# Optimization experiments

Hardware: AMD Instinct MI355X
Metric: run time of the kernel (lower is better)

## Reference

```python
import jax, jax.numpy as jnp
import numpy as np

DROPOUT_RATE = 0.6


def dropout(x, key, rate=DROPOUT_RATE):
    keep = jax.random.bernoulli(key, 1.0 - rate, x.shape)
    return jnp.where(keep, x / (1.0 - rate), 0.0).astype(x.dtype)


def gcn_conv(x, W, b, src, dst, n_nodes):
    # h = x @ W  (tiny linear), then symmetric-normalized scatter-add over edges
    h = x @ W                                             # [N, C_out]
    deg = jax.ops.segment_sum(jnp.ones_like(dst, dtype=h.dtype), dst,
                              num_segments=n_nodes)       # in-degree at targets
    dinv = jnp.where(deg > 0, jax.lax.rsqrt(jnp.maximum(deg, 1.0)), 0.0)
    norm = dinv[src] * dinv[dst]                          # [E]
    msg = h[src] * norm[:, None]                          # [E, C_out] gather
    out = jax.ops.segment_sum(msg, dst, num_segments=n_nodes)  # scatter-add
    return out + b


def setup_inputs() -> dict:
    key = jax.random.key(0)
    k_x, k_e, k_w1, k_w2 = jax.random.split(key, 4)
    N, E = 100000, 6400000
    x = jax.random.normal(k_x, (N, 1), dtype=jnp.float32)
    edge_index = jax.random.randint(k_e, (2, E), 0, N, dtype=jnp.int64)
    # GCNConv weights (glorot-ish scale) and zero biases
    W1 = jax.random.normal(k_w1, (1, 16), dtype=jnp.float32) * (1.0 / np.sqrt(1.0))
    b1 = jnp.zeros((16,), dtype=jnp.float32)
    W2 = jax.random.normal(k_w2, (16, 1), dtype=jnp.float32) * (1.0 / np.sqrt(16.0))
    b2 = jnp.zeros((1,), dtype=jnp.float32)
    return {"x": x, "edge_index": edge_index, "W1": W1, "b1": b1, "W2": W2, "b2": b2}


def reference(x, edge_index, W1, b1, W2, b2):
    n_nodes = x.shape[0]
    src, dst = edge_index[0], edge_index[1]
    k1, k2 = jax.random.split(jax.random.key(42), 2)
    h = dropout(x, k1)
    h = gcn_conv(h, W1, b1, src, dst, n_nodes)
    h = jax.nn.relu(h)
    h = dropout(h, k2)
    out = gcn_conv(h, W2, b2, src, dst, n_nodes)
    return out
```

## Files before the change

### kernel.cpp

```cpp
#include <hip/hip_runtime.h>
#include <hip/hip_bf16.h>
#include <stdint.h>


#define KEEP_P 0.4f
#define RANGE 2048
#define SHIFT 11
#define MASK 2047
#define BPC 512
#define KS 32
#define SEGS (BPC / KS)
#define NBMAX 64

__host__ __device__ inline unsigned rotl32(unsigned v, int s) {
  return (v << s) | (v >> (32 - s));
}

__host__ __device__ inline void threefry2x32(unsigned key0, unsigned key1,
                                             unsigned x0, unsigned x1,
                                             unsigned& o0, unsigned& o1) {
  unsigned ks0 = key0, ks1 = key1, ks2 = key0 ^ key1 ^ 0x1BD11BDAu;
  unsigned v0 = x0 + ks0, v1 = x1 + ks1;
#define TF_R(r) { v0 += v1; v1 = rotl32(v1, r); v1 ^= v0; }
  TF_R(13) TF_R(15) TF_R(26) TF_R(6)
  v0 += ks1; v1 += ks2 + 1u;
  TF_R(17) TF_R(29) TF_R(16) TF_R(24)
  v0 += ks2; v1 += ks0 + 2u;
  TF_R(13) TF_R(15) TF_R(26) TF_R(6)
  v0 += ks0; v1 += ks1 + 3u;
  TF_R(17) TF_R(29) TF_R(16) TF_R(24)
  v0 += ks1; v1 += ks2 + 4u;
  TF_R(13) TF_R(15) TF_R(26) TF_R(6)
  v0 += ks2; v1 += ks0 + 5u;
#undef TF_R
  o0 = v0; o1 = v1;
}

__device__ inline float u01_from_bits(unsigned bits) {
  return __uint_as_float((bits >> 9) | 0x3f800000u) - 1.0f;
}

__global__ __launch_bounds__(256) void k_part(
    const int* __restrict__ src, const int* __restrict__ dst,
    unsigned* __restrict__ slots, unsigned* __restrict__ cnt,
    int NB, int CAP, int e4, int E) {
  __shared__ unsigned cur[NBMAX];
  const int tid = threadIdx.x;
  const size_t blkbase = (size_t)blockIdx.x * NB;
  for (int p = tid; p < NB; p += 256) cur[p] = (unsigned)(p * CAP);
  __syncthreads();
  const int chunk = (e4 + BPC - 1) / BPC;
  const int j0 = blockIdx.x * chunk;
  const int j1 = min(j0 + chunk, e4);
  const int4* dst4 = reinterpret_cast<const int4*>(dst);
  const int4* src4 = reinterpret_cast<const int4*>(src);
  unsigned* myslots = slots + blkbase * CAP;
#define PART_ONE(d, s) { unsigned p = (unsigned)(d) >> SHIFT; \
    unsigned pos = atomicAdd(&cur[p], 1u); \
    myslots[pos] = ((unsigned)(d) & MASK) | ((unsigned)(s) << SHIFT); }
  for (int j = j0 + tid; j < j1; j += 256) {
    int4 d = dst4[j];
    int4 s = src4[j];
    PART_ONE(d.x, s.x) PART_ONE(d.y, s.y) PART_ONE(d.z, s.z) PART_ONE(d.w, s.w)
  }
  if (blockIdx.x == 0) {
    for (int t = e4 * 4 + tid; t < E; t += 256) PART_ONE(dst[t], src[t])
  }
#undef PART_ONE
  __syncthreads();
  for (int p = tid; p < NB; p += 256)
    cnt[blkbase + p] = cur[p] - (unsigned)(p * CAP);
}

__global__ __launch_bounds__(256) void k_deg2(
    const unsigned* __restrict__ slots, const unsigned* __restrict__ cnt,
    unsigned short* __restrict__ part16, int NB, int CAP) {
  __shared__ unsigned bins[RANGE / 2];
  const int tid = threadIdx.x;
  const int p = blockIdx.y, kd = blockIdx.x;
  for (int i = tid; i < RANGE / 2; i += 256) bins[i] = 0u;
  __syncthreads();
  const int b0 = kd * SEGS;
#define DEG_ONE(v) { unsigned r = (v) & MASK; \
    atomicAdd(&bins[r >> 1], 1u << ((r & 1) * 16)); }
  for (int u = 0; u < SEGS / 2; ++u) {
    const int bA = b0 + u, bB = b0 + u + SEGS / 2;
    const int lA = cnt[(size_t)bA * NB + p];
    const int lB = cnt[(size_t)bB * NB + p];
    const unsigned* eA = slots + ((size_t)bA * NB + p) * CAP;
    const unsigned* eB = slots + ((size_t)bB * NB + p) * CAP;
    int jA = tid, jB = tid;
    while (jA < lA && jB < lB) {
      unsigned vA = eA[jA], vB = eB[jB];
      DEG_ONE(vA) DEG_ONE(vB)
      jA += 256; jB += 256;
    }
    for (; jA < lA; jA += 256) DEG_ONE(eA[jA])
    for (; jB < lB; jB += 256) DEG_ONE(eB[jB])
  }
#undef DEG_ONE
  __syncthreads();
  unsigned* my32 = (unsigned*)(part16 + ((size_t)kd * gridDim.y + p) * RANGE);
  for (int i = tid; i < RANGE / 2; i += 256) my32[i] = bins[i];
}

__global__ __launch_bounds__(256) void k_node1(
    const float* __restrict__ x, const unsigned short* __restrict__ part16,
    float* __restrict__ dinv, float* __restrict__ y,
    int NB, int n, unsigned k1a, unsigned k1b) {
  int i = blockIdx.x * blockDim.x + threadIdx.x;
  if (i >= n) return;
  const int p = i >> SHIFT, r = i & MASK;
  unsigned d = 0;
  for (int b = 0; b < KS; ++b)
    d += part16[((size_t)b * NB + p) * RANGE + r];
  float di = (d > 0) ? (1.0f / sqrtf((float)d)) : 0.0f;
  dinv[i] = di;
  unsigned o0, o1;
  threefry2x32(k1a, k1b, 0u, (unsigned)i, o0, o1);
  float u = u01_from_bits(o0 ^ o1);
  float xd = (u < KEEP_P) ? (x[i] / KEEP_P) : 0.0f;
  y[i] = xd * di;
}

__global__ __launch_bounds__(256) void k_scat(
    const unsigned* __restrict__ slots, const unsigned* __restrict__ cnt,
    const float* __restrict__ val, float* __restrict__ part,
    int NB, int CAP) {
  __shared__ float bins[RANGE];
  const int tid = threadIdx.x;
  const int p = blockIdx.y, ks = blockIdx.x;
  for (int i = tid; i < RANGE; i += 256) bins[i] = 0.0f;
  __syncthreads();
  const int b0 = ks * SEGS;
  for (int u = 0; u < SEGS / 2; ++u) {
    const int bA = b0 + u, bB = b0 + u + SEGS / 2;
    const int lA = cnt[(size_t)bA * NB + p];
    const int lB = cnt[(size_t)bB * NB + p];
    const unsigned* eA = slots + ((size_t)bA * NB + p) * CAP;
    const unsigned* eB = slots + ((size_t)bB * NB + p) * CAP;
    int jA = tid, jB = tid;
    while (jA < lA && jB < lB) {
      unsigned vA = eA[jA], vB = eB[jB];
      float aA = val[vA >> SHIFT], aB = val[vB >> SHIFT];
      atomicAdd(&bins[vA & MASK], aA);
      atomicAdd(&bins[vB & MASK], aB);
      jA += 256; jB += 256;
    }
    for (; jA < lA; jA += 256) {
      unsigned v = eA[jA];
      atomicAdd(&bins[v & MASK], val[v >> SHIFT]);
    }
    for (; jB < lB; jB += 256) {
      unsigned v = eB[jB];
      atomicAdd(&bins[v & MASK], val[v >> SHIFT]);
    }
  }
  __syncthreads();
  float* my = part + ((size_t)ks * NB + p) * RANGE;
  for (int i = tid; i < RANGE; i += 256) my[i] = bins[i];
}

__global__ __launch_bounds__(256) void k_node2(
    const float* __restrict__ part, const float* __restrict__ dinv,
    const float* __restrict__ W1, const float* __restrict__ b1,
    const float* __restrict__ W2, float* __restrict__ z2,
    int NB, int n, unsigned k2a, unsigned k2b) {
  int i = blockIdx.x * blockDim.x + threadIdx.x;
  if (i >= n) return;
  const int p = i >> SHIFT, r = i & MASK;
  float s = 0.0f;
  for (int b = 0; b < KS; ++b)
    s += part[((size_t)b * NB + p) * RANGE + r];
  float t = s * dinv[i];
  float z = 0.0f;
  unsigned base = (unsigned)i * 16u;
#pragma unroll
  for (int c = 0; c < 16; ++c) {
    float h = W1[c] * t + b1[c];
    h = fmaxf(h, 0.0f);
    unsigned o0, o1;
    threefry2x32(k2a, k2b, 0u, base + (unsigned)c, o0, o1);
    float u = u01_from_bits(o0 ^ o1);
    float hd = (u < KEEP_P) ? (h / KEEP_P) : 0.0f;
    z += hd * W2[c];
  }
  z2[i] = z * dinv[i];
}

__global__ __launch_bounds__(256) void k_final(
    const float* __restrict__ part, const float* __restrict__ dinv,
    const float* __restrict__ b2, float* __restrict__ out,
    int NB, int n) {
  int i = blockIdx.x * blockDim.x + threadIdx.x;
  if (i >= n) return;
  const int p = i >> SHIFT, r = i & MASK;
  float s = 0.0f;
  for (int b = 0; b < KS; ++b)
    s += part[((size_t)b * NB + p) * RANGE + r];
  out[i] = b2[0] + dinv[i] * s;
}

extern "C" void kernel_launch(void* const* d_in, const int* in_sizes, int n_in,
                              void* d_out, int out_size, void* d_ws, size_t ws_size,
                              hipStream_t stream) {
  const float* x  = (const float*)d_in[0];
  const int* edge = (const int*)d_in[1];
  const float* W1 = (const float*)d_in[2];
  const float* b1 = (const float*)d_in[3];
  const float* W2 = (const float*)d_in[4];
  const float* b2 = (const float*)d_in[5];
  float* out = (float*)d_out;

  const int N = in_sizes[0];
  const int E = in_sizes[1] / 2;
  const int* src = edge;
  const int* dst = edge + E;

  const int NP = (N + 255) & ~255;
  const int NB = (N + RANGE - 1) / RANGE;

  const size_t cnt_sz  = (size_t)BPC * NB * 4;
  const size_t part_sz = (size_t)KS * NB * RANGE * 4;
  const size_t small_sz = (size_t)3 * NP * 4;
  size_t fixed = cnt_sz + part_sz + small_sz + 512;
  size_t avail = ws_size > fixed ? ws_size - fixed : 0;
  int CAP = (int)(avail / ((size_t)NB * BPC * 4));
  if (CAP > 512) CAP = 512;
  if (CAP < 288) CAP = 288;

  char* w = (char*)d_ws;
  unsigned* slots = (unsigned*)w;        w += (size_t)NB * BPC * CAP * 4;
  unsigned* cnt   = (unsigned*)w;        w += cnt_sz;
  w = (char*)(((uintptr_t)w + 255) & ~(uintptr_t)255);
  float* part_f = (float*)w;
  unsigned short* part16 = (unsigned short*)w;
  w += part_sz;
  float* dinv = (float*)w;
  float* y    = dinv + NP;
  float* z2   = y + NP;

  unsigned k1a, k1b, k2a, k2b;
  threefry2x32(0u, 42u, 0u, 0u, k1a, k1b);
  threefry2x32(0u, 42u, 0u, 1u, k2a, k2b);

  const int e4 = E >> 2;
  const int gN = (N + 255) / 256;

  k_part <<<BPC, 256, 0, stream>>>(src, dst, slots, cnt, NB, CAP, e4, E);
  k_deg2 <<<dim3(KS, NB), 256, 0, stream>>>(slots, cnt, part16, NB, CAP);
  k_node1<<<gN, 256, 0, stream>>>(x, part16, dinv, y, NB, N, k1a, k1b);
  k_scat <<<dim3(KS, NB), 256, 0, stream>>>(slots, cnt, y, part_f, NB, CAP);
  k_node2<<<gN, 256, 0, stream>>>(part_f, dinv, W1, b1, W2, z2, NB, N, k2a, k2b);
  k_scat <<<dim3(KS, NB), 256, 0, stream>>>(slots, cnt, z2, part_f, NB, CAP);
  k_final<<<gN, 256, 0, stream>>>(part_f, dinv, b2, out, NB, N);
}
```

Before: 231.5 us.

## Stage partition writes through shared-memory tiles and assign segments per wavefront

The partition kernel now handles edges in tiles of 2048. For each tile it builds a per-bucket histogram, scans it, sorts the tile into shared memory, and then writes each bucket's run to global memory as a contiguous sequence, replacing the old scattered per-edge global stores. The degree and scatter kernels now give each wavefront its own segments and read slot entries with 16-byte vector loads, and CAP is rounded down to a multiple of 4 so those loads stay aligned. The cost is extra syncthreads and shared-memory traffic in the partition kernel, plus possible load imbalance between wavefronts.

```diff
diff --git a/kernel.cpp b/kernel.cpp
--- a/kernel.cpp
+++ b/kernel.cpp
@@ -11,6 +11,8 @@
 #define KS 32
 #define SEGS (BPC / KS)
 #define NBMAX 64
+#define TILE 2048
+#define TILE4 (TILE / 4)
 
 __host__ __device__ inline unsigned rotl32(unsigned v, int s) {
   return (v << s) | (v >> (32 - s));
@@ -44,29 +46,83 @@
     const int* __restrict__ src, const int* __restrict__ dst,
     unsigned* __restrict__ slots, unsigned* __restrict__ cnt,
     int NB, int CAP, int e4, int E) {
-  __shared__ unsigned cur[NBMAX];
+  __shared__ unsigned hist[NBMAX], scan_s[NBMAX + 1], off[NBMAX];
+  __shared__ unsigned tbase[NBMAX], cur[NBMAX];
+  __shared__ unsigned stage[TILE];
+  __shared__ unsigned char stage_p[TILE];
   const int tid = threadIdx.x;
   const size_t blkbase = (size_t)blockIdx.x * NB;
+  unsigned* myslots = slots + blkbase * CAP;
   for (int p = tid; p < NB; p += 256) cur[p] = (unsigned)(p * CAP);
-  __syncthreads();
   const int chunk = (e4 + BPC - 1) / BPC;
   const int j0 = blockIdx.x * chunk;
   const int j1 = min(j0 + chunk, e4);
   const int4* dst4 = reinterpret_cast<const int4*>(dst);
   const int4* src4 = reinterpret_cast<const int4*>(src);
-  unsigned* myslots = slots + blkbase * CAP;
-#define PART_ONE(d, s) { unsigned p = (unsigned)(d) >> SHIFT; \
-    unsigned pos = atomicAdd(&cur[p], 1u); \
-    myslots[pos] = ((unsigned)(d) & MASK) | ((unsigned)(s) << SHIFT); }
-  for (int j = j0 + tid; j < j1; j += 256) {
-    int4 d = dst4[j];
-    int4 s = src4[j];
-    PART_ONE(d.x, s.x) PART_ONE(d.y, s.y) PART_ONE(d.z, s.z) PART_ONE(d.w, s.w)
-  }
+
+  for (int t0 = j0; t0 < j1; t0 += TILE4) {
+    __syncthreads();
+    for (int p = tid; p < NB; p += 256) hist[p] = 0u;
+    __syncthreads();
+    const int ja = t0 + tid, jb = t0 + TILE4 / 2 + tid;
+    const bool va = ja < j1 && tid < TILE4 / 2;
+    const bool vb = jb < j1;
+    int4 da, db;
+    if (va) {
+      da = dst4[ja];
+      atomicAdd(&hist[(unsigned)da.x >> SHIFT], 1u);
+      atomicAdd(&hist[(unsigned)da.y >> SHIFT], 1u);
+      atomicAdd(&hist[(unsigned)da.z >> SHIFT], 1u);
+      atomicAdd(&hist[(unsigned)da.w >> SHIFT], 1u);
+    }
+    if (vb) {
+      db = dst4[jb];
+      atomicAdd(&hist[(unsigned)db.x >> SHIFT], 1u);
+      atomicAdd(&hist[(unsigned)db.y >> SHIFT], 1u);
+      atomicAdd(&hist[(unsigned)db.z >> SHIFT], 1u);
+      atomicAdd(&hist[(unsigned)db.w >> SHIFT], 1u);
+    }
+    __syncthreads();
+    if (tid == 0) {
+      unsigned acc = 0;
+      for (int p = 0; p < NB; ++p) { scan_s[p] = acc; acc += hist[p]; }
+      scan_s[NB] = acc;
+    }
+    __syncthreads();
+    for (int p = tid; p < NB; p += 256) {
+      off[p] = scan_s[p];
+      tbase[p] = cur[p];
+      cur[p] += hist[p];
+    }
+    __syncthreads();
+#define STAGE1(d, s) { unsigned ud = (unsigned)(d), us = (unsigned)(s); \
+    unsigned p = ud >> SHIFT; unsigned pos = atomicAdd(&off[p], 1u); \
+    stage[pos] = (ud & MASK) | (us << SHIFT); stage_p[pos] = (unsigned char)p; }
+    if (va) {
+      int4 sa = src4[ja];
+      STAGE1(da.x, sa.x) STAGE1(da.y, sa.y) STAGE1(da.z, sa.z) STAGE1(da.w, sa.w)
+    }
+    if (vb) {
+      int4 sb = src4[jb];
+      STAGE1(db.x, sb.x) STAGE1(db.y, sb.y) STAGE1(db.z, sb.z) STAGE1(db.w, sb.w)
+    }
+#undef STAGE1
+    __syncthreads();
+    const int tc = (int)scan_s[NB];
+    for (int i = tid; i < tc; i += 256) {
+      unsigned p = stage_p[i];
+      myslots[tbase[p] + ((unsigned)i - scan_s[p])] = stage[i];
+    }
+  }
+  __syncthreads();
   if (blockIdx.x == 0) {
-    for (int t = e4 * 4 + tid; t < E; t += 256) PART_ONE(dst[t], src[t])
-  }
-#undef PART_ONE
+    for (int t = e4 * 4 + tid; t < E; t += 256) {
+      unsigned ud = (unsigned)dst[t], us = (unsigned)src[t];
+      unsigned p = ud >> SHIFT;
+      unsigned pos = atomicAdd(&cur[p], 1u);
+      myslots[pos] = (ud & MASK) | (us << SHIFT);
+    }
+  }
   __syncthreads();
   for (int p = tid; p < NB; p += 256)
     cnt[blkbase + p] = cur[p] - (unsigned)(p * CAP);
@@ -76,27 +132,34 @@
     const unsigned* __restrict__ slots, const unsigned* __restrict__ cnt,
     unsigned short* __restrict__ part16, int NB, int CAP) {
   __shared__ unsigned bins[RANGE / 2];
-  const int tid = threadIdx.x;
+  const int tid = threadIdx.x, w = tid >> 6, lane = tid & 63;
   const int p = blockIdx.y, kd = blockIdx.x;
   for (int i = tid; i < RANGE / 2; i += 256) bins[i] = 0u;
   __syncthreads();
   const int b0 = kd * SEGS;
 #define DEG_ONE(v) { unsigned r = (v) & MASK; \
     atomicAdd(&bins[r >> 1], 1u << ((r & 1) * 16)); }
-  for (int u = 0; u < SEGS / 2; ++u) {
-    const int bA = b0 + u, bB = b0 + u + SEGS / 2;
+  for (int q = 0; q < 4; q += 2) {
+    const int bA = b0 + w + 4 * q, bB = b0 + w + 4 * (q + 1);
     const int lA = cnt[(size_t)bA * NB + p];
     const int lB = cnt[(size_t)bB * NB + p];
     const unsigned* eA = slots + ((size_t)bA * NB + p) * CAP;
     const unsigned* eB = slots + ((size_t)bB * NB + p) * CAP;
-    int jA = tid, jB = tid;
-    while (jA < lA && jB < lB) {
-      unsigned vA = eA[jA], vB = eB[jB];
-      DEG_ONE(vA) DEG_ONE(vB)
-      jA += 256; jB += 256;
-    }
-    for (; jA < lA; jA += 256) DEG_ONE(eA[jA])
-    for (; jB < lB; jB += 256) DEG_ONE(eB[jB])
+    const int lmax = lA > lB ? lA : lB;
+    for (int base = 4 * lane; base < lmax; base += 256) {
+      if (base + 4 <= lA) {
+        uint4 av = *reinterpret_cast<const uint4*>(eA + base);
+        DEG_ONE(av.x) DEG_ONE(av.y) DEG_ONE(av.z) DEG_ONE(av.w)
+      } else {
+        for (int k = base; k < lA; ++k) DEG_ONE(eA[k])
+      }
+      if (base + 4 <= lB) {
+        uint4 bv = *reinterpret_cast<const uint4*>(eB + base);
+        DEG_ONE(bv.x) DEG_ONE(bv.y) DEG_ONE(bv.z) DEG_ONE(bv.w)
+      } else {
+        for (int k = base; k < lB; ++k) DEG_ONE(eB[k])
+      }
+    }
   }
 #undef DEG_ONE
   __syncthreads();
@@ -128,32 +191,65 @@
     const float* __restrict__ val, float* __restrict__ part,
     int NB, int CAP) {
   __shared__ float bins[RANGE];
-  const int tid = threadIdx.x;
+  const int tid = threadIdx.x, w = tid >> 6, lane = tid & 63;
   const int p = blockIdx.y, ks = blockIdx.x;
   for (int i = tid; i < RANGE; i += 256) bins[i] = 0.0f;
   __syncthreads();
   const int b0 = ks * SEGS;
-  for (int u = 0; u < SEGS / 2; ++u) {
-    const int bA = b0 + u, bB = b0 + u + SEGS / 2;
+  for (int q = 0; q < 4; q += 2) {
+    const int bA = b0 + w + 4 * q, bB = b0 + w + 4 * (q + 1);
     const int lA = cnt[(size_t)bA * NB + p];
     const int lB = cnt[(size_t)bB * NB + p];
     const unsigned* eA = slots + ((size_t)bA * NB + p) * CAP;
     const unsigned* eB = slots + ((size_t)bB * NB + p) * CAP;
-    int jA = tid, jB = tid;
-    while (jA < lA && jB < lB) {
-      unsigned vA = eA[jA], vB = eB[jB];
-      float aA = val[vA >> SHIFT], aB = val[vB >> SHIFT];
-      atomicAdd(&bins[vA & MASK], aA);
-      atomicAdd(&bins[vB & MASK], aB);
-      jA += 256; jB += 256;
-    }
-    for (; jA < lA; jA += 256) {
-      unsigned v = eA[jA];
-      atomicAdd(&bins[v & MASK], val[v >> SHIFT]);
-    }
-    for (; jB < lB; jB += 256) {
-      unsigned v = eB[jB];
-      atomicAdd(&bins[v & MASK], val[v >> SHIFT]);
+    const int lmax = lA > lB ? lA : lB;
+    for (int base = 4 * lane; base < lmax; base += 256) {
+      const bool fA = base + 4 <= lA, fB = base + 4 <= lB;
+      if (fA && fB) {
+        uint4 av = *reinterpret_cast<const uint4*>(eA + base);
+        uint4 bv = *reinterpret_cast<const uint4*>(eB + base);
+        float a0 = val[av.x >> SHIFT], a1 = val[av.y >> SHIFT];
+        float a2 = val[av.z >> SHIFT], a3 = val[av.w >> SHIFT];
+        float c0 = val[bv.x >> SHIFT], c1 = val[bv.y >> SHIFT];
+        float c2 = val[bv.z >> SHIFT], c3 = val[bv.w >> SHIFT];
+        atomicAdd(&bins[av.x & MASK], a0);
+        atomicAdd(&bins[av.y & MASK], a1);
+        atomicAdd(&bins[av.z & MASK], a2);
+        atomicAdd(&bins[av.w & MASK], a3);
+        atomicAdd(&bins[bv.x & MASK], c0);
+        atomicAdd(&bins[bv.y & MASK], c1);
+        atomicAdd(&bins[bv.z & MASK], c2);
+        atomicAdd(&bins[bv.w & MASK], c3);
+      } else {
+        if (fA) {
+          uint4 av = *reinterpret_cast<const uint4*>(eA + base);
+          float a0 = val[av.x >> SHIFT], a1 = val[av.y >> SHIFT];
+          float a2 = val[av.z >> SHIFT], a3 = val[av.w >> SHIFT];
+          atomicAdd(&bins[av.x & MASK], a0);
+          atomicAdd(&bins[av.y & MASK], a1);
+          atomicAdd(&bins[av.z & MASK], a2);
+          atomicAdd(&bins[av.w & MASK], a3);
+        } else {
+          for (int k = base; k < lA; ++k) {
+            unsigned v = eA[k];
+            atomicAdd(&bins[v & MASK], val[v >> SHIFT]);
+          }
+        }
+        if (fB) {
+          uint4 bv = *reinterpret_cast<const uint4*>(eB + base);
+          float c0 = val[bv.x >> SHIFT], c1 = val[bv.y >> SHIFT];
+          float c2 = val[bv.z >> SHIFT], c3 = val[bv.w >> SHIFT];
+          atomicAdd(&bins[bv.x & MASK], c0);
+          atomicAdd(&bins[bv.y & MASK], c1);
+          atomicAdd(&bins[bv.z & MASK], c2);
+          atomicAdd(&bins[bv.w & MASK], c3);
+        } else {
+          for (int k = base; k < lB; ++k) {
+            unsigned v = eB[k];
+            atomicAdd(&bins[v & MASK], val[v >> SHIFT]);
+          }
+        }
+      }
     }
   }
   __syncthreads();
@@ -226,6 +322,7 @@
   size_t fixed = cnt_sz + part_sz + small_sz + 512;
   size_t avail = ws_size > fixed ? ws_size - fixed : 0;
   int CAP = (int)(avail / ((size_t)NB * BPC * 4));
+  CAP &= ~3;
   if (CAP > 512) CAP = 512;
   if (CAP < 288) CAP = 288;
 
```

Result: faster. 225.7 us (-2.5%).
